# Performance work log

Measured on AMD Instinct MI355X. Metric: run time of the kernel, lower is better.

The kernel has to match this reference:

```python
import jax, jax.numpy as jnp
import numpy as np
from jax.scipy.linalg import expm

N_MODES, N_LAYERS, CUTOFF, BATCH = 6, 6, 3, 1024
M2 = N_MODES * (N_MODES - 1) // 2                  # beamsplitter thetas per interferometer
N_IF = N_MODES * (N_MODES - 1) + (N_MODES - 1)     # interferometer param count = 35

_np_a = np.diag(np.sqrt(np.arange(1, CUTOFF)), 1)  # truncated annihilation operator
A = jnp.asarray(_np_a, jnp.complex64)
AD = A.conj().T
NVEC = jnp.arange(CUTOFF, dtype=jnp.float32)       # number operator diagonal
X_OP = A + AD                                      # x quadrature (hbar=2, PennyLane/SF convention)
BS_GEN = jnp.kron(AD, A) - jnp.kron(A, AD)         # Beamsplitter(theta, 0) generator
SQ_GEN = A @ A - AD @ AD                           # Squeezing(r, 0) generator (times r/2)
D_GEN = AD - A                                     # Displacement(r, 0) generator

def disp_gate(r):
    return expm(r.astype(jnp.complex64) * D_GEN)

def sq_gate(r):
    return expm(0.5 * r.astype(jnp.complex64) * SQ_GEN)

def bs_gate(theta):
    return expm(theta.astype(jnp.complex64) * BS_GEN)

def apply_1(psi, U, m):
    # psi: (B, D, ..., D); apply DxD gate U on mode m
    psi = jnp.moveaxis(psi, 1 + m, -1)
    psi = psi @ U.T
    return jnp.moveaxis(psi, -1, 1 + m)

def apply_1_batched(psi, U, m):
    # U: (B, D, D) per-sample gate (data-encoding displacement)
    psi = jnp.moveaxis(psi, 1 + m, -1)
    psi = jnp.einsum('b...j,bij->b...i', psi, U)
    return jnp.moveaxis(psi, -1, 1 + m)

def apply_2(psi, U, m):
    psi = jnp.moveaxis(psi, (1 + m, 2 + m), (-2, -1))
    sh = psi.shape
    psi = (psi.reshape(sh[:-2] + (CUTOFF * CUTOFF,)) @ U.T).reshape(sh)
    return jnp.moveaxis(psi, (-2, -1), (1 + m, 2 + m))

def apply_diag(psi, d, m):
    shape = [1] * psi.ndim
    shape[1 + m] = CUTOFF
    return psi * d.reshape(shape)

def interferometer(psi, params):
    theta = params[:M2]
    rphi = params[-N_MODES:]  # faithful to source: overlaps last (unused) phi param
    n = 0
    for l in range(N_MODES):
        for k in range(N_MODES - 1):
            if (l + k) % 2 != 1:
                psi = apply_2(psi, bs_gate(theta[n]), k)
                n += 1
    for i in range(max(1, N_MODES - 1)):
        psi = apply_diag(psi, jnp.exp(1j * rphi[i] * NVEC), i)
    return psi

def cv_forward(x, theta_1, theta_2, squeezing_r, displacement_r, kerr_params):
    B = x.shape[0]
    psi = jnp.zeros((B,) + (CUTOFF,) * N_MODES, jnp.complex64)
    psi = psi.at[(slice(None),) + (0,) * N_MODES].set(1.0)  # |0...0> vacuum
    for m in range(N_MODES):  # data-encoding displacements, per-sample gates
        psi = apply_1_batched(psi, jax.vmap(disp_gate)(x[:, m]), m)
    for L in range(N_LAYERS):
        psi = interferometer(psi, theta_1[L])
        for m in range(N_MODES):
            psi = apply_1(psi, sq_gate(squeezing_r[L, m] * 0.5), m)
        psi = interferometer(psi, theta_2[L])
        for m in range(N_MODES):
            psi = apply_1(psi, disp_gate(displacement_r[L, m]), m)
            psi = apply_diag(psi, jnp.exp(1j * (kerr_params[L, m] * 0.001) * NVEC * NVEC), m)
    sum_axes = tuple(range(1, psi.ndim))
    outs = [jnp.sum(jnp.conj(psi) * apply_1(psi, X_OP, m), axis=sum_axes).real
            for m in range(N_MODES)]
    return jnp.stack(outs, axis=1)  # (B, N_MODES)

def setup_inputs() -> dict:
    key = jax.random.key(0)
    ks = jax.random.split(key, 6)
    passive_sd = 0.01 * np.pi
    return {
        'x': jax.random.normal(ks[0], (BATCH, N_MODES), jnp.float32),
        'theta_1': jax.random.normal(ks[1], (N_LAYERS, N_IF), jnp.float32) * passive_sd,
        'theta_2': jax.random.normal(ks[2], (N_LAYERS, N_IF), jnp.float32) * np.float32(0.2 * np.pi),
        'squeezing_r': jax.random.normal(ks[3], (N_LAYERS, N_MODES), jnp.float32) * 1e-3,
        'displacement_r': jax.random.normal(ks[4], (N_LAYERS, N_MODES), jnp.float32) * 1e-3,
        'kerr_params': jax.random.normal(ks[5], (N_LAYERS, N_MODES), jnp.float32) * 1e-3,
    }

def reference(x, theta_1, theta_2, squeezing_r, displacement_r, kerr_params):
    return cv_forward(x, theta_1, theta_2, squeezing_r, displacement_r, kerr_params)
```

## Files before the change

kernel.cpp:

```cpp
#include <hip/hip_runtime.h>

#define SQRT2f 1.41421356237309515f
#define SQRT3f 1.73205080756887729f

__device__ __forceinline__ float2 cmul(float2 a, float2 b) {
  return make_float2(a.x*b.x - a.y*b.y, a.x*b.y + a.y*b.x);
}
__device__ __forceinline__ float2 cadd(float2 a, float2 b) {
  return make_float2(a.x + b.x, a.y + b.y);
}

template<int SP>
__device__ __forceinline__ void bs_nonet(float2* __restrict__ psi, int base,
                                         float2 cs) {
  const float c = cs.x, s = cs.y;
  const float c2 = c*c - s*s, s2 = 2.f*c*s;
  const float cc = c*c, ss = s*s, rcs = SQRT2f*c*s;
  float2 a1 = psi[base+SP],   a3 = psi[base+3*SP];
  float2 a2 = psi[base+2*SP], a4 = psi[base+4*SP], a6 = psi[base+6*SP];
  float2 a5 = psi[base+5*SP], a7 = psi[base+7*SP];
  psi[base+SP]   = make_float2(c*a1.x - s*a3.x, c*a1.y - s*a3.y);
  psi[base+3*SP] = make_float2(s*a1.x + c*a3.x, s*a1.y + c*a3.y);
  psi[base+2*SP] = make_float2(cc*a2.x - rcs*a4.x + ss*a6.x,
                               cc*a2.y - rcs*a4.y + ss*a6.y);
  psi[base+4*SP] = make_float2(rcs*a2.x + c2*a4.x - rcs*a6.x,
                               rcs*a2.y + c2*a4.y - rcs*a6.y);
  psi[base+6*SP] = make_float2(ss*a2.x + rcs*a4.x + cc*a6.x,
                               ss*a2.y + rcs*a4.y + cc*a6.y);
  psi[base+5*SP] = make_float2(c2*a5.x - s2*a7.x, c2*a5.y - s2*a7.y);
  psi[base+7*SP] = make_float2(s2*a5.x + c2*a7.x, s2*a5.y + c2*a7.y);
}

template<int SP>
__device__ __forceinline__ void sqf_nonet(float2* __restrict__ psi, int base,
                                          const float2* __restrict__ A) {
  float2 A00=A[0],A02=A[1],A11=A[2],A20=A[3],A22=A[4];
  float2 B00=A[5],B02=A[6],B11=A[7],B20=A[8],B22=A[9];
  float2 v[3][3];
#pragma unroll
  for (int j = 0; j < 3; ++j)
#pragma unroll
    for (int jb = 0; jb < 3; ++jb) v[j][jb] = psi[base + j*3*SP + jb*SP];
  float2 t[3][3];
#pragma unroll
  for (int j = 0; j < 3; ++j) {
    t[j][0] = cadd(cmul(B00,v[j][0]), cmul(B02,v[j][2]));
    t[j][1] = cmul(B11,v[j][1]);
    t[j][2] = cadd(cmul(B20,v[j][0]), cmul(B22,v[j][2]));
  }
#pragma unroll
  for (int ib = 0; ib < 3; ++ib) {
    psi[base + ib*SP]        = cadd(cmul(A00,t[0][ib]), cmul(A02,t[2][ib]));
    psi[base + 3*SP + ib*SP] = cmul(A11,t[1][ib]);
    psi[base + 6*SP + ib*SP] = cadd(cmul(A20,t[0][ib]), cmul(A22,t[2][ib]));
  }
}

template<int SP>
__device__ __forceinline__ void dpf_nonet(float2* __restrict__ psi, int base,
                                          const float2* __restrict__ A) {
  const float2* Bm = A + 9;
  float2 v[3][3];
#pragma unroll
  for (int j = 0; j < 3; ++j)
#pragma unroll
    for (int jb = 0; jb < 3; ++jb) v[j][jb] = psi[base + j*3*SP + jb*SP];
  float2 t[3][3];
#pragma unroll
  for (int j = 0; j < 3; ++j)
#pragma unroll
    for (int ib = 0; ib < 3; ++ib)
      t[j][ib] = cadd(cadd(cmul(Bm[ib*3+0],v[j][0]), cmul(Bm[ib*3+1],v[j][1])),
                      cmul(Bm[ib*3+2],v[j][2]));
#pragma unroll
  for (int i = 0; i < 3; ++i)
#pragma unroll
    for (int ib = 0; ib < 3; ++ib)
      psi[base + i*3*SP + ib*SP] =
        cadd(cadd(cmul(A[i*3+0],t[0][ib]), cmul(A[i*3+1],t[1][ib])),
             cmul(A[i*3+2],t[2][ib]));
}

#define BASE4(g, s0,s1,s2,s3) ({ int _d=(g); int _b=(_d%3)*(s0); _d/=3; \
  _b += (_d%3)*(s1); _d/=3; _b += (_d%3)*(s2); _d/=3; _b += (_d%3)*(s3); _b; })
#define BASE5(g, s0,s1,s2,s3,s4) ({ int _d=(g); int _b=(_d%3)*(s0); _d/=3; \
  _b += (_d%3)*(s1); _d/=3; _b += (_d%3)*(s2); _d/=3; _b += (_d%3)*(s3); _d/=3; \
  _b += (_d%3)*(s4); _b; })

__global__ __launch_bounds__(128)
void cvnn_kernel(const float* __restrict__ x,
                 const float* __restrict__ th1,
                 const float* __restrict__ th2,
                 const float* __restrict__ sr,
                 const float* __restrict__ dr,
                 const float* __restrict__ kp,
                 float* __restrict__ out) {
  __shared__ float2 psi[729];
  __shared__ float2 gtab[690];
  __shared__ float red[12];

  const int tid = threadIdx.x;
  const int bidx = blockIdx.x;

  for (int f = tid; f < 690; f += 128) {
    float sn, cn; float2 v;
    if (f < 180) {
      int L = f/30, r2 = f%30, pass = r2/15, n = r2%15;
      float th = (pass ? th2 : th1)[L*35 + n];
      sincosf(th, &sn, &cn); v = make_float2(cn, sn);
    } else if (f < 360) {
      int idx = f - 180; int Lm = idx/5, e = idx%5;
      int L = Lm/6, mode = Lm%6;
      float Sq, Cq; sincosf(0.25f*SQRT2f*sr[L*6+mode], &Sq, &Cq);
      float2 ph = make_float2(1.f, 0.f);
      if (mode < 5) { float ps, pc; sincosf(th1[L*35+29+mode], &ps, &pc);
                      ph = make_float2(pc, ps); }
      float2 ph2 = cmul(ph, ph);
      if      (e == 0) v = make_float2(Cq, 0.f);
      else if (e == 1) v = make_float2(Sq*ph2.x, Sq*ph2.y);
      else if (e == 2) v = ph;
      else if (e == 3) v = make_float2(-Sq, 0.f);
      else             v = make_float2(Cq*ph2.x, Cq*ph2.y);
    } else if (f < 684) {
      int idx = f - 360; int Lm = idx/9, e = idx%9;
      int L = Lm/6, mode = Lm%6; int i = e/3, j = e%3;
      sincosf(SQRT3f*dr[L*6+mode], &sn, &cn);
      float sw = sn*(1.f/SQRT3f), cw = (1.f-cn)*(1.f/3.f);
      float U;
      if      (i==0) U = (j==0) ? (1.f-cw)     : (j==1) ? (-sw)         : (SQRT2f*cw);
      else if (i==1) U = (j==0) ? (sw)         : (j==1) ? (1.f-3.f*cw)  : (-SQRT2f*sw);
      else           U = (j==0) ? (SQRT2f*cw)  : (j==1) ? (SQRT2f*sw)   : (1.f-2.f*cw);
      float2 ph = make_float2(1.f, 0.f);
      if (mode < 5) { float ps, pc; sincosf(th2[L*35+29+mode], &ps, &pc);
                      ph = make_float2(pc, ps); }
      float2 phj = (j==0) ? make_float2(1.f,0.f) : (j==1) ? ph : cmul(ph, ph);
      float ks, kc; sincosf(0.001f*kp[L*6+mode], &ks, &kc);
      float2 k1 = make_float2(kc, ks);
      float2 ki = (i==0) ? make_float2(1.f,0.f)
                : (i==1) ? k1 : cmul(cmul(k1,k1), cmul(k1,k1));
      float2 t = cmul(phj, ki);
      v = make_float2(U*t.x, U*t.y);
    } else {
      int mode = f - 684;
      sincosf(SQRT3f*x[bidx*6 + mode], &sn, &cn);
      v = make_float2(sn*(1.f/SQRT3f), (1.f-cn)*(1.f/3.f));
    }
    gtab[f] = v;
  }
  __syncthreads();

  for (int idx = tid; idx < 729; idx += 128) {
    float pr = 1.f; int d = idx;
#pragma unroll
    for (int mm = 5; mm >= 0; --mm) {
      int n = d % 3; d /= 3;
      float2 dc = gtab[684 + mm];
      pr *= (n==0) ? (1.f-dc.y) : (n==1) ? dc.x : SQRT2f*dc.y;
    }
    psi[idx] = make_float2(pr, 0.f);
  }

  const bool act = (tid < 81);
  const int g = (tid < 81) ? tid : 0;
  const int b0 = g;
  const int b1 = BASE4(g, 1, 3, 9, 243);
  const int b2 = BASE4(g, 1, 3, 81, 243);
  const int b3 = BASE4(g, 1, 27, 81, 243);
  const int b4 = BASE4(g, 9, 27, 81, 243);
  __syncthreads();

#define BSSWEEP(SP, BB, IDX) { if (act) { float2 cs_ = gtab[IDX]; \
    bs_nonet<SP>(psi, BB, cs_); } __syncthreads(); }
#define SQSWEEP(SP, BB, LL, m) { if (act) { \
    const float2* A_ = &gtab[180 + ((LL)*6+(m))*5]; \
    sqf_nonet<SP>(psi, BB, A_); } __syncthreads(); }
#define DPSWEEP(SP, BB, LL, m) { if (act) { \
    const float2* A_ = &gtab[360 + ((LL)*6+(m))*9]; \
    dpf_nonet<SP>(psi, BB, A_); } __syncthreads(); }

  for (int L = 0; L < 6; ++L) {
    {
      const int o = L*30;
      BSSWEEP(81, b0, o+0);  BSSWEEP(9, b2, o+1);  BSSWEEP(1, b4, o+2);
      BSSWEEP(27, b1, o+3);  BSSWEEP(3, b3, o+4);
      BSSWEEP(81, b0, o+5);  BSSWEEP(9, b2, o+6);  BSSWEEP(1, b4, o+7);
      BSSWEEP(27, b1, o+8);  BSSWEEP(3, b3, o+9);
      BSSWEEP(81, b0, o+10); BSSWEEP(9, b2, o+11); BSSWEEP(1, b4, o+12);
      BSSWEEP(27, b1, o+13); BSSWEEP(3, b3, o+14);
      SQSWEEP(81, b0, L, 0); SQSWEEP(9, b2, L, 2); SQSWEEP(1, b4, L, 4);
    }
    {
      const int o = L*30 + 15;
      BSSWEEP(81, b0, o+0);  BSSWEEP(9, b2, o+1);  BSSWEEP(1, b4, o+2);
      BSSWEEP(27, b1, o+3);  BSSWEEP(3, b3, o+4);
      BSSWEEP(81, b0, o+5);  BSSWEEP(9, b2, o+6);  BSSWEEP(1, b4, o+7);
      BSSWEEP(27, b1, o+8);  BSSWEEP(3, b3, o+9);
      BSSWEEP(81, b0, o+10); BSSWEEP(9, b2, o+11); BSSWEEP(1, b4, o+12);
      BSSWEEP(27, b1, o+13); BSSWEEP(3, b3, o+14);
      DPSWEEP(81, b0, L, 0); DPSWEEP(9, b2, L, 2); DPSWEEP(1, b4, L, 4);
    }
  }

  float xs[6] = {0.f, 0.f, 0.f, 0.f, 0.f, 0.f};
  for (int it = 0; it < 2; ++it) {
    int t = tid + (it << 7);
    if (t < 243) {
#define XACC(m, SS, BB) { int b_ = (BB); \
      float2 a_ = psi[b_]; float2 b2_ = psi[b_+(SS)]; float2 c_ = psi[b_+2*(SS)]; \
      xs[m] += 2.f*(a_.x*b2_.x + a_.y*b2_.y) + 2.f*SQRT2f*(b2_.x*c_.x + b2_.y*c_.y); }
      XACC(0, 243, BASE5(t, 1, 3, 9, 27, 81));
      XACC(1, 81,  BASE5(t, 1, 3, 9, 27, 243));
      XACC(2, 27,  BASE5(t, 1, 3, 9, 81, 243));
      XACC(3, 9,   BASE5(t, 1, 3, 27, 81, 243));
      XACC(4, 3,   BASE5(t, 1, 9, 27, 81, 243));
      XACC(5, 1,   BASE5(t, 3, 9, 27, 81, 243));
    }
  }
  const int lane = tid & 63, wid = tid >> 6;
#pragma unroll
  for (int m = 0; m < 6; ++m) {
    float v = xs[m];
    for (int off = 32; off > 0; off >>= 1) v += __shfl_down(v, off);
    if (lane == 0) red[wid*6 + m] = v;
  }
  __syncthreads();
  if (tid < 6) out[bidx*6 + tid] = red[tid] + red[6 + tid];
}

extern "C" void kernel_launch(void* const* d_in, const int* in_sizes, int n_in,
                              void* d_out, int out_size, void* d_ws, size_t ws_size,
                              hipStream_t stream) {
  const float* x  = (const float*)d_in[0];
  const float* t1 = (const float*)d_in[1];
  const float* t2 = (const float*)d_in[2];
  const float* sr = (const float*)d_in[3];
  const float* dr = (const float*)d_in[4];
  const float* kp = (const float*)d_in[5];
  const int B = in_sizes[0] / 6;
  cvnn_kernel<<<B, 128, 0, stream>>>(x, t1, t2, sr, dr, kp, (float*)d_out);
}
```

Measured before the change: 99.72 us.

## Fuse displacement and squeeze gates into adjacent beamsplitters, fold final layer into observable

Each displacement and squeeze gate is merged with the beamsplitter that follows it on the same mode pair, so both run in one pass over shared-memory psi and one barrier is removed per fused pair. The last layer's displacement/phase/Kerr gates are no longer applied to the state. Instead they are folded into a per-mode 3x3 Hermitian observable M = D^dagger X D, precomputed in the gate table, and the expectation is computed as a quadratic form. Beamsplitter coefficients are also prefetched into a register one sweep ahead. Together these remove about a sixth of the barrier-separated sweeps, at the cost of more register pressure and a heavier table setup and reduction.

```diff
diff --git a/kernel.cpp b/kernel.cpp
--- a/kernel.cpp
+++ b/kernel.cpp
@@ -8,6 +8,20 @@
 }
 __device__ __forceinline__ float2 cadd(float2 a, float2 b) {
   return make_float2(a.x + b.x, a.y + b.y);
+}
+
+__device__ __forceinline__ void bs_q(float2 q[9], float2 cs) {
+  const float c = cs.x, s = cs.y;
+  const float c2 = c*c - s*s, s2 = 2.f*c*s;
+  const float cc = c*c, ss = s*s, rcs = SQRT2f*c*s;
+  float2 a1=q[1], a3=q[3], a2=q[2], a4=q[4], a6=q[6], a5=q[5], a7=q[7];
+  q[1] = make_float2(c*a1.x - s*a3.x, c*a1.y - s*a3.y);
+  q[3] = make_float2(s*a1.x + c*a3.x, s*a1.y + c*a3.y);
+  q[2] = make_float2(cc*a2.x - rcs*a4.x + ss*a6.x, cc*a2.y - rcs*a4.y + ss*a6.y);
+  q[4] = make_float2(rcs*a2.x + c2*a4.x - rcs*a6.x, rcs*a2.y + c2*a4.y - rcs*a6.y);
+  q[6] = make_float2(ss*a2.x + rcs*a4.x + cc*a6.x, ss*a2.y + rcs*a4.y + cc*a6.y);
+  q[5] = make_float2(c2*a5.x - s2*a7.x, c2*a5.y - s2*a7.y);
+  q[7] = make_float2(s2*a5.x + c2*a7.x, s2*a5.y + c2*a7.y);
 }
 
 template<int SP>
@@ -32,10 +46,42 @@
 }
 
 template<int SP>
-__device__ __forceinline__ void sqf_nonet(float2* __restrict__ psi, int base,
-                                          const float2* __restrict__ A) {
-  float2 A00=A[0],A02=A[1],A11=A[2],A20=A[3],A22=A[4];
-  float2 B00=A[5],B02=A[6],B11=A[7],B20=A[8],B22=A[9];
+__device__ __forceinline__ void dpbs_nonet(float2* __restrict__ psi, int base,
+                                           const float2* __restrict__ G,
+                                           float2 cs) {
+  const float2* A = G; const float2* B = G + 9;
+  float2 v[3][3];
+#pragma unroll
+  for (int j = 0; j < 3; ++j)
+#pragma unroll
+    for (int jb = 0; jb < 3; ++jb) v[j][jb] = psi[base + j*3*SP + jb*SP];
+  float2 t[3][3];
+#pragma unroll
+  for (int j = 0; j < 3; ++j)
+#pragma unroll
+    for (int ib = 0; ib < 3; ++ib)
+      t[j][ib] = cadd(cadd(cmul(B[ib*3+0],v[j][0]), cmul(B[ib*3+1],v[j][1])),
+                      cmul(B[ib*3+2],v[j][2]));
+  float2 q[9];
+#pragma unroll
+  for (int i = 0; i < 3; ++i)
+#pragma unroll
+    for (int ib = 0; ib < 3; ++ib)
+      q[i*3+ib] = cadd(cadd(cmul(A[i*3+0],t[0][ib]), cmul(A[i*3+1],t[1][ib])),
+                       cmul(A[i*3+2],t[2][ib]));
+  bs_q(q, cs);
+#pragma unroll
+  for (int i = 0; i < 3; ++i)
+#pragma unroll
+    for (int ib = 0; ib < 3; ++ib) psi[base + i*3*SP + ib*SP] = q[i*3+ib];
+}
+
+template<int SP>
+__device__ __forceinline__ void sqbs_nonet(float2* __restrict__ psi, int base,
+                                           const float2* __restrict__ G,
+                                           float2 cs) {
+  float2 A00=G[0],A02=G[1],A11=G[2],A20=G[3],A22=G[4];
+  float2 B00=G[5],B02=G[6],B11=G[7],B20=G[8],B22=G[9];
   float2 v[3][3];
 #pragma unroll
   for (int j = 0; j < 3; ++j)
@@ -48,37 +94,18 @@
     t[j][1] = cmul(B11,v[j][1]);
     t[j][2] = cadd(cmul(B20,v[j][0]), cmul(B22,v[j][2]));
   }
+  float2 q[9];
 #pragma unroll
   for (int ib = 0; ib < 3; ++ib) {
-    psi[base + ib*SP]        = cadd(cmul(A00,t[0][ib]), cmul(A02,t[2][ib]));
-    psi[base + 3*SP + ib*SP] = cmul(A11,t[1][ib]);
-    psi[base + 6*SP + ib*SP] = cadd(cmul(A20,t[0][ib]), cmul(A22,t[2][ib]));
-  }
-}
-
-template<int SP>
-__device__ __forceinline__ void dpf_nonet(float2* __restrict__ psi, int base,
-                                          const float2* __restrict__ A) {
-  const float2* Bm = A + 9;
-  float2 v[3][3];
-#pragma unroll
-  for (int j = 0; j < 3; ++j)
-#pragma unroll
-    for (int jb = 0; jb < 3; ++jb) v[j][jb] = psi[base + j*3*SP + jb*SP];
-  float2 t[3][3];
-#pragma unroll
-  for (int j = 0; j < 3; ++j)
-#pragma unroll
-    for (int ib = 0; ib < 3; ++ib)
-      t[j][ib] = cadd(cadd(cmul(Bm[ib*3+0],v[j][0]), cmul(Bm[ib*3+1],v[j][1])),
-                      cmul(Bm[ib*3+2],v[j][2]));
+    q[ib]   = cadd(cmul(A00,t[0][ib]), cmul(A02,t[2][ib]));
+    q[3+ib] = cmul(A11,t[1][ib]);
+    q[6+ib] = cadd(cmul(A20,t[0][ib]), cmul(A22,t[2][ib]));
+  }
+  bs_q(q, cs);
 #pragma unroll
   for (int i = 0; i < 3; ++i)
 #pragma unroll
-    for (int ib = 0; ib < 3; ++ib)
-      psi[base + i*3*SP + ib*SP] =
-        cadd(cadd(cmul(A[i*3+0],t[0][ib]), cmul(A[i*3+1],t[1][ib])),
-             cmul(A[i*3+2],t[2][ib]));
+    for (int ib = 0; ib < 3; ++ib) psi[base + i*3*SP + ib*SP] = q[i*3+ib];
 }
 
 #define BASE4(g, s0,s1,s2,s3) ({ int _d=(g); int _b=(_d%3)*(s0); _d/=3; \
@@ -86,6 +113,28 @@
 #define BASE5(g, s0,s1,s2,s3,s4) ({ int _d=(g); int _b=(_d%3)*(s0); _d/=3; \
   _b += (_d%3)*(s1); _d/=3; _b += (_d%3)*(s2); _d/=3; _b += (_d%3)*(s3); _d/=3; \
   _b += (_d%3)*(s4); _b; })
+
+__device__ __forceinline__ float2 dpk_entry(const float* __restrict__ dr,
+                                            const float* __restrict__ th2,
+                                            const float* __restrict__ kp,
+                                            int L, int mode, int i, int j) {
+  float sn, cn; sincosf(SQRT3f*dr[L*6+mode], &sn, &cn);
+  float sw = sn*(1.f/SQRT3f), cw = (1.f-cn)*(1.f/3.f);
+  float U;
+  if      (i==0) U = (j==0) ? (1.f-cw)     : (j==1) ? (-sw)         : (SQRT2f*cw);
+  else if (i==1) U = (j==0) ? (sw)         : (j==1) ? (1.f-3.f*cw)  : (-SQRT2f*sw);
+  else           U = (j==0) ? (SQRT2f*cw)  : (j==1) ? (SQRT2f*sw)   : (1.f-2.f*cw);
+  float2 ph = make_float2(1.f, 0.f);
+  if (mode < 5) { float ps, pc; sincosf(th2[L*35+29+mode], &ps, &pc);
+                  ph = make_float2(pc, ps); }
+  float2 phj = (j==0) ? make_float2(1.f,0.f) : (j==1) ? ph : cmul(ph, ph);
+  float ks, kc; sincosf(0.001f*kp[L*6+mode], &ks, &kc);
+  float2 k1 = make_float2(kc, ks);
+  float2 ki = (i==0) ? make_float2(1.f,0.f)
+            : (i==1) ? k1 : cmul(cmul(k1,k1), cmul(k1,k1));
+  float2 t = cmul(phj, ki);
+  return make_float2(U*t.x, U*t.y);
+}
 
 __global__ __launch_bounds__(128)
 void cvnn_kernel(const float* __restrict__ x,
@@ -105,41 +154,46 @@
   for (int f = tid; f < 690; f += 128) {
     float sn, cn; float2 v;
     if (f < 180) {
-      int L = f/30, r2 = f%30, pass = r2/15, n = r2%15;
-      float th = (pass ? th2 : th1)[L*35 + n];
+      int Lp = f/15, pos = f%15;
+      int L = Lp/2, pass = Lp%2;
+      float th = (pass ? th2 : th1)[L*35 + pos];
       sincosf(th, &sn, &cn); v = make_float2(cn, sn);
     } else if (f < 360) {
-      int idx = f - 180; int Lm = idx/5, e = idx%5;
-      int L = Lm/6, mode = Lm%6;
+      int i = f - 180; int Lc = i/10, e = i%10;
+      int L = Lc/3, c3 = Lc%3;
+      int mode = 2*c3 + (e >= 5); int ee = e%5;
       float Sq, Cq; sincosf(0.25f*SQRT2f*sr[L*6+mode], &Sq, &Cq);
       float2 ph = make_float2(1.f, 0.f);
       if (mode < 5) { float ps, pc; sincosf(th1[L*35+29+mode], &ps, &pc);
                       ph = make_float2(pc, ps); }
       float2 ph2 = cmul(ph, ph);
-      if      (e == 0) v = make_float2(Cq, 0.f);
-      else if (e == 1) v = make_float2(Sq*ph2.x, Sq*ph2.y);
-      else if (e == 2) v = ph;
-      else if (e == 3) v = make_float2(-Sq, 0.f);
-      else             v = make_float2(Cq*ph2.x, Cq*ph2.y);
+      if      (ee == 0) v = make_float2(Cq, 0.f);
+      else if (ee == 1) v = make_float2(Sq*ph2.x, Sq*ph2.y);
+      else if (ee == 2) v = ph;
+      else if (ee == 3) v = make_float2(-Sq, 0.f);
+      else              v = make_float2(Cq*ph2.x, Cq*ph2.y);
+    } else if (f < 630) {
+      int i = f - 360; int Ld = i/18, e = i%18;
+      int Ls = Ld/3, c3 = Ld%3;
+      int mode = 2*c3 + (e >= 9); int ee = e%9;
+      v = dpk_entry(dr, th2, kp, Ls, mode, ee/3, ee%3);
     } else if (f < 684) {
-      int idx = f - 360; int Lm = idx/9, e = idx%9;
-      int L = Lm/6, mode = Lm%6; int i = e/3, j = e%3;
-      sincosf(SQRT3f*dr[L*6+mode], &sn, &cn);
-      float sw = sn*(1.f/SQRT3f), cw = (1.f-cn)*(1.f/3.f);
-      float U;
-      if      (i==0) U = (j==0) ? (1.f-cw)     : (j==1) ? (-sw)         : (SQRT2f*cw);
-      else if (i==1) U = (j==0) ? (sw)         : (j==1) ? (1.f-3.f*cw)  : (-SQRT2f*sw);
-      else           U = (j==0) ? (SQRT2f*cw)  : (j==1) ? (SQRT2f*sw)   : (1.f-2.f*cw);
-      float2 ph = make_float2(1.f, 0.f);
-      if (mode < 5) { float ps, pc; sincosf(th2[L*35+29+mode], &ps, &pc);
-                      ph = make_float2(pc, ps); }
-      float2 phj = (j==0) ? make_float2(1.f,0.f) : (j==1) ? ph : cmul(ph, ph);
-      float ks, kc; sincosf(0.001f*kp[L*6+mode], &ks, &kc);
-      float2 k1 = make_float2(kc, ks);
-      float2 ki = (i==0) ? make_float2(1.f,0.f)
-                : (i==1) ? k1 : cmul(cmul(k1,k1), cmul(k1,k1));
-      float2 t = cmul(phj, ki);
-      v = make_float2(U*t.x, U*t.y);
+      int i = f - 630; int m = i/9, e = i%9;
+      int ii = e/3, jj = e%3;
+      float2 D0i = dpk_entry(dr, th2, kp, 5, m, 0, ii);
+      float2 D1i = dpk_entry(dr, th2, kp, 5, m, 1, ii);
+      float2 D2i = dpk_entry(dr, th2, kp, 5, m, 2, ii);
+      float2 D0j = dpk_entry(dr, th2, kp, 5, m, 0, jj);
+      float2 D1j = dpk_entry(dr, th2, kp, 5, m, 1, jj);
+      float2 D2j = dpk_entry(dr, th2, kp, 5, m, 2, jj);
+      float2 c0 = make_float2(D0i.x, -D0i.y);
+      float2 c1 = make_float2(D1i.x, -D1i.y);
+      float2 c2 = make_float2(D2i.x, -D2i.y);
+      float2 acc = cmul(c0, D1j);
+      float2 tmp = make_float2(D0j.x + SQRT2f*D2j.x, D0j.y + SQRT2f*D2j.y);
+      acc = cadd(acc, cmul(c1, tmp));
+      acc = cadd(acc, cmul(c2, make_float2(SQRT2f*D1j.x, SQRT2f*D1j.y)));
+      v = acc;
     } else {
       int mode = f - 684;
       sincosf(SQRT3f*x[bidx*6 + mode], &sn, &cn);
@@ -169,36 +223,39 @@
   const int b4 = BASE4(g, 9, 27, 81, 243);
   __syncthreads();
 
-#define BSSWEEP(SP, BB, IDX) { if (act) { float2 cs_ = gtab[IDX]; \
-    bs_nonet<SP>(psi, BB, cs_); } __syncthreads(); }
-#define SQSWEEP(SP, BB, LL, m) { if (act) { \
-    const float2* A_ = &gtab[180 + ((LL)*6+(m))*5]; \
-    sqf_nonet<SP>(psi, BB, A_); } __syncthreads(); }
-#define DPSWEEP(SP, BB, LL, m) { if (act) { \
-    const float2* A_ = &gtab[360 + ((LL)*6+(m))*9]; \
-    dpf_nonet<SP>(psi, BB, A_); } __syncthreads(); }
-
+  float2 csN = gtab[0];
+  __syncthreads();
+
+#define BSP(SP, BB, NEXT)  { if (act) bs_nonet<SP>(psi, BB, csN); \
+    csN = gtab[NEXT]; __syncthreads(); }
+#define DPBS(SP, BB, GI, NEXT) { if (act) dpbs_nonet<SP>(psi, BB, &gtab[GI], csN); \
+    csN = gtab[NEXT]; __syncthreads(); }
+#define SQBS(SP, BB, GI, NEXT) { if (act) sqbs_nonet<SP>(psi, BB, &gtab[GI], csN); \
+    csN = gtab[NEXT]; __syncthreads(); }
+
+#pragma unroll
   for (int L = 0; L < 6; ++L) {
+    const int i1 = (L*2)*15, i2 = (L*2+1)*15;
+    if (L == 0) {
+      BSP(81, b0, i1+1); BSP(9, b2, i1+2); BSP(1, b4, i1+3);
+    } else {
+      const int gd = 360 + (L-1)*3*18;
+      DPBS(81, b0, gd+0,  i1+1); DPBS(9, b2, gd+18, i1+2); DPBS(1, b4, gd+36, i1+3);
+    }
+    BSP(27, b1, i1+4);  BSP(3, b3, i1+5);
+    BSP(81, b0, i1+6);  BSP(9, b2, i1+7);  BSP(1, b4, i1+8);
+    BSP(27, b1, i1+9);  BSP(3, b3, i1+10);
+    BSP(81, b0, i1+11); BSP(9, b2, i1+12); BSP(1, b4, i1+13);
+    BSP(27, b1, i1+14); BSP(3, b3, i2+0);
     {
-      const int o = L*30;
-      BSSWEEP(81, b0, o+0);  BSSWEEP(9, b2, o+1);  BSSWEEP(1, b4, o+2);
-      BSSWEEP(27, b1, o+3);  BSSWEEP(3, b3, o+4);
-      BSSWEEP(81, b0, o+5);  BSSWEEP(9, b2, o+6);  BSSWEEP(1, b4, o+7);
-      BSSWEEP(27, b1, o+8);  BSSWEEP(3, b3, o+9);
-      BSSWEEP(81, b0, o+10); BSSWEEP(9, b2, o+11); BSSWEEP(1, b4, o+12);
-      BSSWEEP(27, b1, o+13); BSSWEEP(3, b3, o+14);
-      SQSWEEP(81, b0, L, 0); SQSWEEP(9, b2, L, 2); SQSWEEP(1, b4, L, 4);
-    }
-    {
-      const int o = L*30 + 15;
-      BSSWEEP(81, b0, o+0);  BSSWEEP(9, b2, o+1);  BSSWEEP(1, b4, o+2);
-      BSSWEEP(27, b1, o+3);  BSSWEEP(3, b3, o+4);
-      BSSWEEP(81, b0, o+5);  BSSWEEP(9, b2, o+6);  BSSWEEP(1, b4, o+7);
-      BSSWEEP(27, b1, o+8);  BSSWEEP(3, b3, o+9);
-      BSSWEEP(81, b0, o+10); BSSWEEP(9, b2, o+11); BSSWEEP(1, b4, o+12);
-      BSSWEEP(27, b1, o+13); BSSWEEP(3, b3, o+14);
-      DPSWEEP(81, b0, L, 0); DPSWEEP(9, b2, L, 2); DPSWEEP(1, b4, L, 4);
-    }
+      const int gs = 180 + L*3*10;
+      SQBS(81, b0, gs+0, i2+1); SQBS(9, b2, gs+10, i2+2); SQBS(1, b4, gs+20, i2+3);
+    }
+    BSP(27, b1, i2+4);  BSP(3, b3, i2+5);
+    BSP(81, b0, i2+6);  BSP(9, b2, i2+7);  BSP(1, b4, i2+8);
+    BSP(27, b1, i2+9);  BSP(3, b3, i2+10);
+    BSP(81, b0, i2+11); BSP(9, b2, i2+12); BSP(1, b4, i2+13);
+    BSP(27, b1, i2+14); BSP(3, b3, (L < 5) ? (L+1)*30 : 0);
   }
 
   float xs[6] = {0.f, 0.f, 0.f, 0.f, 0.f, 0.f};
@@ -206,8 +263,15 @@
     int t = tid + (it << 7);
     if (t < 243) {
 #define XACC(m, SS, BB) { int b_ = (BB); \
-      float2 a_ = psi[b_]; float2 b2_ = psi[b_+(SS)]; float2 c_ = psi[b_+2*(SS)]; \
-      xs[m] += 2.f*(a_.x*b2_.x + a_.y*b2_.y) + 2.f*SQRT2f*(b2_.x*c_.x + b2_.y*c_.y); }
+      float2 a_ = psi[b_]; float2 e_ = psi[b_+(SS)]; float2 f_ = psi[b_+2*(SS)]; \
+      const float2* M_ = &gtab[630 + (m)*9]; \
+      float d0 = M_[0].x, d1 = M_[4].x, d2 = M_[8].x; \
+      float2 M01 = M_[1], M02 = M_[2], M12 = M_[5]; \
+      xs[m] += d0*(a_.x*a_.x + a_.y*a_.y) + d1*(e_.x*e_.x + e_.y*e_.y) \
+             + d2*(f_.x*f_.x + f_.y*f_.y) \
+        + 2.f*(M01.x*(a_.x*e_.x + a_.y*e_.y) - M01.y*(a_.x*e_.y - a_.y*e_.x)) \
+        + 2.f*(M02.x*(a_.x*f_.x + a_.y*f_.y) - M02.y*(a_.x*f_.y - a_.y*f_.x)) \
+        + 2.f*(M12.x*(e_.x*f_.x + e_.y*f_.y) - M12.y*(e_.x*f_.y - e_.y*f_.x)); }
       XACC(0, 243, BASE5(t, 1, 3, 9, 27, 81));
       XACC(1, 81,  BASE5(t, 1, 3, 9, 27, 243));
       XACC(2, 27,  BASE5(t, 1, 3, 9, 81, 243));
```

Result: faster. 92.86 us (-6.9%).
